# Kernel tuning notes

Measured on AMD Instinct MI355X. Metric: run time of the kernel, lower is better.

The kernel has to match this reference:

```python
import jax, jax.numpy as jnp
import numpy as np
import math

ATTN_SCALE = 1.0 / math.sqrt(128.0)
NEG_INF = float(np.finfo(np.float32).min)


def get_slopes(n_heads: int) -> np.ndarray:
    # ALiBi head-specific slopes, geometric series; handles non-power-of-2 heads.
    n = 2 ** math.floor(math.log2(n_heads))
    m_0 = 2.0 ** (-8.0 / n)
    m = m_0 ** np.arange(1, 1 + n, dtype=np.float64)
    if n < n_heads:
        m_hat_0 = 2.0 ** (-4.0 / n)
        m_hat = m_hat_0 ** np.arange(1, 1 + 2 * (n_heads - n), 2, dtype=np.float64)
        m = np.concatenate([m, m_hat])
    return m.astype(np.float32).reshape(1, -1, 1, 1)  # [1, h, 1, 1]


def setup_inputs() -> dict:
    key = jax.random.key(0)
    kq, kk, kv = jax.random.split(key, 3)
    b, h, s, d = 4, 16, 2048, 128
    q = jax.random.normal(kq, (b, h, s, d), dtype=jnp.float32)
    k = jax.random.normal(kk, (b, h, s, d), dtype=jnp.float32)
    v = jax.random.normal(kv, (b, h, s, d), dtype=jnp.float32)
    return {"q": q, "k": k, "v": v}


def reference(q, k, v):
    b, h, s_q, d = q.shape
    s_kv = k.shape[2]
    # scores: [b, h, s_q, s_kv]
    s = jnp.einsum('bhqd,bhkd->bhqk', q, k) * ATTN_SCALE
    # ALiBi: (j - i) * slope_h, added after scaling
    rel = (jnp.arange(s_kv, dtype=q.dtype)[None, :]
           - jnp.arange(s_q, dtype=q.dtype)[:, None])  # [s_q, s_kv]
    slopes = jnp.asarray(get_slopes(h), dtype=q.dtype)  # [1, h, 1, 1]
    s = s + rel[None, None, :, :] * slopes
    # causal mask: positions j > i get -inf
    causal = jnp.arange(s_kv)[None, :] > jnp.arange(s_q)[:, None]  # [s_q, s_kv]
    s = jnp.where(causal[None, None, :, :], jnp.array(-jnp.inf, dtype=s.dtype), s)
    p = jax.nn.softmax(s, axis=-1)
    o = jnp.einsum('bhqk,bhkd->bhqd', p, v)
    return o
```

## Files before the change

kernel.cpp:

```cpp
#include <hip/hip_runtime.h>
#include <math.h>

#define S_LEN 2048
#define DHEAD 128
#define NHEAD 16
#define QBLK  256
#define KVBLK 64
#define ATT_SCALE 0.08838834764831845f
#define LOG2E 1.4426950408889634f
#define SHIFT2 11.5f

#define KP 136
#define VP 72

typedef __attribute__((ext_vector_type(4))) float f32x4;
typedef __attribute__((ext_vector_type(8))) short s16x8;
typedef __attribute__((ext_vector_type(2))) int   i32x2;

__device__ __forceinline__ int pk2(float lo, float hi) {
  int d;
  asm("v_cvt_pk_bf16_f32 %0, %1, %2" : "=v"(d) : "v"(lo), "v"(hi));
  return d;
}

#define BARRIER() do {                                   \
    asm volatile("s_waitcnt lgkmcnt(0)" ::: "memory");   \
    __builtin_amdgcn_s_barrier();                        \
  } while (0)


__global__ __launch_bounds__(512, 2)
void alibi_attn_fwd(const float* __restrict__ Qg, const float* __restrict__ Kg,
                    const float* __restrict__ Vg, float* __restrict__ Og)
{
  __shared__ __align__(16) short kt[2][KVBLK * KP];
  __shared__ __align__(16) short vt[2][DHEAD * VP];

  const int tid  = threadIdx.x;
  const int lane = tid & 63;
  const int w    = tid >> 6;
  const int l16  = lane & 15;
  const int lg   = lane >> 4;

  const int n    = blockIdx.x;
  const int bh   = n & 63;
  const int p    = n >> 6;
  const int head = bh & (NHEAD - 1);

  const size_t base = (size_t)bh * S_LEN * DHEAD;
  const float* Q = Qg + base;
  const float* K = Kg + base;
  const float* V = Vg + base;
  float*       O = Og + base;

  const float slope2 = exp2f(-0.5f * (float)(head + 1)) * LOG2E;
  float cn16[4], rsv[4];
  #pragma unroll
  for (int x = 0; x < 4; ++x) { cn16[x] = (float)(16 * x) * slope2; rsv[x] = (float)x * slope2; }

  s16x8 ones;
  #pragma unroll
  for (int jj = 0; jj < 8; ++jj) ones[jj] = (short)0x3f80;

  const f32x4 zero4 = {0.f, 0.f, 0.f, 0.f};

  const int qt0 = 7 - p, qt1 = p;
  const int qb0 = qt0 * QBLK, qb1 = qt1 * QBLK;
  const int n0  = 4 * (qt0 + 1);
  const int NT  = n0 + 4 * (qt1 + 1);

  const int kr  = tid >> 3;
  const int d0k = 16 * (tid & 7);
  const int grp = tid & 15, vnt = grp >> 2, vg = grp & 3;
  const int Rv  = 16 * vnt + 4 * vg;
  const int dv  = 4 * (tid >> 4);
  const int vslotb = 32 * (vnt >> 1) + 8 * vg + 4 * (vnt & 1);

  f32x4 ka[4], va[4];

#define LOAD_TILE(KV0) do {                                            \
    const float* kp_ = K + (size_t)((KV0) + kr) * DHEAD + d0k;         \
    ka[0] = *(const f32x4*)(kp_);      ka[1] = *(const f32x4*)(kp_ + 4);  \
    ka[2] = *(const f32x4*)(kp_ + 8);  ka[3] = *(const f32x4*)(kp_ + 12); \
    const float* vp_ = V + (size_t)((KV0) + Rv) * DHEAD + dv;          \
    va[0] = *(const f32x4*)(vp_);                                      \
    va[1] = *(const f32x4*)(vp_ + DHEAD);                              \
    va[2] = *(const f32x4*)(vp_ + 2*DHEAD);                            \
    va[3] = *(const f32x4*)(vp_ + 3*DHEAD);                            \
  } while (0)

#define STORE_TILE(B) do {                                             \
    short* ktp = &kt[B][kr * KP + d0k];                                \
    union { int d[4]; s16x8 v; } u0, u1;                               \
    u0.d[0] = pk2(ka[0][0], ka[0][1]); u0.d[1] = pk2(ka[0][2], ka[0][3]); \
    u0.d[2] = pk2(ka[1][0], ka[1][1]); u0.d[3] = pk2(ka[1][2], ka[1][3]); \
    u1.d[0] = pk2(ka[2][0], ka[2][1]); u1.d[1] = pk2(ka[2][2], ka[2][3]); \
    u1.d[2] = pk2(ka[3][0], ka[3][1]); u1.d[3] = pk2(ka[3][2], ka[3][3]); \
    *(s16x8*)(ktp)     = u0.v;                                         \
    *(s16x8*)(ktp + 8) = u1.v;                                         \
    _Pragma("unroll")                                                  \
    for (int e = 0; e < 4; ++e) {                                      \
      i32x2 dvv;                                                       \
      dvv[0] = pk2(va[0][e], va[1][e]);                                \
      dvv[1] = pk2(va[2][e], va[3][e]);                                \
      *(i32x2*)&vt[B][(dv + e) * VP + vslotb] = dvv;                   \
    }                                                                  \
  } while (0)

  s16x8 qf[2][4];
  f32x4 oacc[2][8], lacc[2];
  int   iq0 = 0;
  int   qb  = qb0;

  auto init_phase = [&](int qbn) {
    qb  = qbn;
    iq0 = qbn + 32 * w + l16;
    #pragma unroll
    for (int m = 0; m < 2; ++m) {
      const float* qp = Q + (size_t)(qbn + 32*w + 16*m + l16) * DHEAD + 8*lg;
      #pragma unroll
      for (int c = 0; c < 4; ++c) {
        f32x4 a = *(const f32x4*)(qp + 32*c);
        f32x4 b = *(const f32x4*)(qp + 32*c + 4);
        const float sc = ATT_SCALE * LOG2E;
        union { int d[4]; s16x8 v; } uu;
        uu.d[0] = pk2(a[0]*sc, a[1]*sc); uu.d[1] = pk2(a[2]*sc, a[3]*sc);
        uu.d[2] = pk2(b[0]*sc, b[1]*sc); uu.d[3] = pk2(b[2]*sc, b[3]*sc);
        qf[m][c] = uu.v;
      }
      #pragma unroll
      for (int dt = 0; dt < 8; ++dt) oacc[m][dt] = zero4;
      lacc[m] = zero4;
    }
  };

  auto epilogue = [&](int qbn) {
    #pragma unroll
    for (int m = 0; m < 2; ++m) {
      #pragma unroll
      for (int r = 0; r < 4; ++r) {
        const float inv = 1.0f / lacc[m][r];
        float* op = O + (size_t)(qbn + 32*w + 16*m + 4*lg + r) * DHEAD + l16;
        #pragma unroll
        for (int dt = 0; dt < 8; ++dt) op[dt * 16] = oacc[m][dt][r] * inv;
      }
    }
  };

  init_phase(qb0);
  LOAD_TILE(0);
  STORE_TILE(0);
  LOAD_TILE(KVBLK);
  __syncthreads();

  for (int s = 0; s < NT; ++s) {
    if (s == n0) { epilogue(qb0); init_phase(qb1); }
    const int cur = s & 1;
    const int kv0 = ((s < n0) ? s : s - n0) * KVBLK;
    const bool active = (kv0 <= qb + 32 * w + 31);
    const short* ktc = kt[cur];
    const short* vtc = vt[cur];

    f32x4 sacc[2][4];
    if (active) {
      #pragma unroll
      for (int nt = 0; nt < 4; ++nt) { sacc[0][nt] = zero4; sacc[1][nt] = zero4; }
      __builtin_amdgcn_s_setprio(1);
      #pragma unroll
      for (int c = 0; c < 4; ++c) {
        #pragma unroll
        for (int nt = 0; nt < 4; ++nt) {
          s16x8 kf = *(const s16x8*)&ktc[(nt*16 + l16) * KP + 32*c + 8*lg];
          sacc[0][nt] = __builtin_amdgcn_mfma_f32_16x16x32_bf16(kf, qf[0][c], sacc[0][nt], 0, 0, 0);
          sacc[1][nt] = __builtin_amdgcn_mfma_f32_16x16x32_bf16(kf, qf[1][c], sacc[1][nt], 0, 0, 0);
        }
      }
      __builtin_amdgcn_s_setprio(0);
    }

    if (s + 1 < NT) STORE_TILE((s + 1) & 1);
    if (s + 2 < NT) {
      const int s2 = s + 2;
      LOAD_TILE(((s2 < n0) ? s2 : s2 - n0) * KVBLK);
    }

    if (active) {
      const bool needMask = (kv0 + KVBLK - 1 > qb + 32 * w);
      s16x8 pa[2][2];
      #pragma unroll
      for (int m = 0; m < 2; ++m) {
        const int dji = kv0 + 4*lg - (iq0 + 16*m);
        const float b0m = (float)dji * slope2 - SHIFT2;
        float pv[4][4];
        #pragma unroll
        for (int nt = 0; nt < 4; ++nt) {
          const float bmn = b0m + cn16[nt];
          #pragma unroll
          for (int r = 0; r < 4; ++r)
            pv[nt][r] = __builtin_amdgcn_exp2f(sacc[m][nt][r] + bmn + rsv[r]);
        }
        if (needMask) {
          #pragma unroll
          for (int nt = 0; nt < 4; ++nt)
            #pragma unroll
            for (int r = 0; r < 4; ++r)
              if (dji + 16*nt + r > 0) pv[nt][r] = 0.f;
        }
        #pragma unroll
        for (int c2 = 0; c2 < 2; ++c2) {
          union { int d[4]; s16x8 v; } uu;
          uu.d[0] = pk2(pv[2*c2][0],   pv[2*c2][1]);
          uu.d[1] = pk2(pv[2*c2][2],   pv[2*c2][3]);
          uu.d[2] = pk2(pv[2*c2+1][0], pv[2*c2+1][1]);
          uu.d[3] = pk2(pv[2*c2+1][2], pv[2*c2+1][3]);
          pa[m][c2] = uu.v;
        }
      }

      __builtin_amdgcn_s_setprio(1);
      #pragma unroll
      for (int c2 = 0; c2 < 2; ++c2) {
        lacc[0] = __builtin_amdgcn_mfma_f32_16x16x32_bf16(pa[0][c2], ones, lacc[0], 0, 0, 0);
        lacc[1] = __builtin_amdgcn_mfma_f32_16x16x32_bf16(pa[1][c2], ones, lacc[1], 0, 0, 0);
        #pragma unroll
        for (int dt = 0; dt < 8; ++dt) {
          s16x8 bv = *(const s16x8*)&vtc[(dt*16 + l16) * VP + c2*32 + 8*lg];
          oacc[0][dt] = __builtin_amdgcn_mfma_f32_16x16x32_bf16(pa[0][c2], bv, oacc[0][dt], 0, 0, 0);
          oacc[1][dt] = __builtin_amdgcn_mfma_f32_16x16x32_bf16(pa[1][c2], bv, oacc[1][dt], 0, 0, 0);
        }
      }
      __builtin_amdgcn_s_setprio(0);
    }

    BARRIER();
  }
  epilogue(qb1);
}

extern "C" void kernel_launch(void* const* d_in, const int* in_sizes, int n_in,
                              void* d_out, int out_size, void* d_ws, size_t ws_size,
                              hipStream_t stream) {
  (void)in_sizes; (void)n_in; (void)out_size; (void)d_ws; (void)ws_size;
  const float* q = (const float*)d_in[0];
  const float* k = (const float*)d_in[1];
  const float* v = (const float*)d_in[2];
  float* o = (float*)d_out;
  dim3 grid(256);
  dim3 block(512);
  alibi_attn_fwd<<<grid, block, 0, stream>>>(q, k, v, o);
}
```

Baseline: 110.1 us.

## Software-pipeline PV matmul one tile behind QK with triple-buffered V

Defers the P·V MFMA block for tile s-1 until after the QK and exp computation for tile s, so the MFMA work of one stage can overlap the exp/convert VALU work of the next. V shared memory moves from double to triple buffering to keep the previous tile's V alive, and the shared-memory store of the next tile now happens at the start of each iteration. The extra V buffer raises LDS use and carried P fragments raise register pressure, which may affect the two-blocks-per-CU occupancy target.

```diff
diff --git a/kernel.cpp b/kernel.cpp
--- a/kernel.cpp
+++ b/kernel.cpp
@@ -34,7 +34,7 @@
                     const float* __restrict__ Vg, float* __restrict__ Og)
 {
   __shared__ __align__(16) short kt[2][KVBLK * KP];
-  __shared__ __align__(16) short vt[2][DHEAD * VP];
+  __shared__ __align__(16) short vt[3][DHEAD * VP];
 
   const int tid  = threadIdx.x;
   const int lane = tid & 63;
@@ -89,8 +89,8 @@
     va[3] = *(const f32x4*)(vp_ + 3*DHEAD);                            \
   } while (0)
 
-#define STORE_TILE(B) do {                                             \
-    short* ktp = &kt[B][kr * KP + d0k];                                \
+#define STORE_TILE(BK, BV) do {                                        \
+    short* ktp = &kt[BK][kr * KP + d0k];                               \
     union { int d[4]; s16x8 v; } u0, u1;                               \
     u0.d[0] = pk2(ka[0][0], ka[0][1]); u0.d[1] = pk2(ka[0][2], ka[0][3]); \
     u0.d[2] = pk2(ka[1][0], ka[1][1]); u0.d[3] = pk2(ka[1][2], ka[1][3]); \
@@ -103,7 +103,7 @@
       i32x2 dvv;                                                       \
       dvv[0] = pk2(va[0][e], va[1][e]);                                \
       dvv[1] = pk2(va[2][e], va[3][e]);                                \
-      *(i32x2*)&vt[B][(dv + e) * VP + vslotb] = dvv;                   \
+      *(i32x2*)&vt[BV][(dv + e) * VP + vslotb] = dvv;                  \
     }                                                                  \
   } while (0)
 
@@ -147,22 +147,48 @@
     }
   };
 
+  s16x8 pa[2][2];
+  bool  pactive = false;
+
+  auto pv_block = [&](const short* vtc) {
+    __builtin_amdgcn_s_setprio(1);
+    #pragma unroll
+    for (int c2 = 0; c2 < 2; ++c2) {
+      lacc[0] = __builtin_amdgcn_mfma_f32_16x16x32_bf16(pa[0][c2], ones, lacc[0], 0, 0, 0);
+      lacc[1] = __builtin_amdgcn_mfma_f32_16x16x32_bf16(pa[1][c2], ones, lacc[1], 0, 0, 0);
+      #pragma unroll
+      for (int dt = 0; dt < 8; ++dt) {
+        s16x8 bv = *(const s16x8*)&vtc[(dt*16 + l16) * VP + c2*32 + 8*lg];
+        oacc[0][dt] = __builtin_amdgcn_mfma_f32_16x16x32_bf16(pa[0][c2], bv, oacc[0][dt], 0, 0, 0);
+        oacc[1][dt] = __builtin_amdgcn_mfma_f32_16x16x32_bf16(pa[1][c2], bv, oacc[1][dt], 0, 0, 0);
+      }
+    }
+    __builtin_amdgcn_s_setprio(0);
+  };
+
   init_phase(qb0);
   LOAD_TILE(0);
-  STORE_TILE(0);
+  STORE_TILE(0, 0);
   LOAD_TILE(KVBLK);
   __syncthreads();
 
   for (int s = 0; s < NT; ++s) {
-    if (s == n0) { epilogue(qb0); init_phase(qb1); }
-    const int cur = s & 1;
+    if (s == n0) {
+      if (pactive) pv_block(vt[(n0 - 1) % 3]);
+      epilogue(qb0);
+      init_phase(qb1);
+      pactive = false;
+    }
     const int kv0 = ((s < n0) ? s : s - n0) * KVBLK;
+
+    if (s + 1 < NT) STORE_TILE((s + 1) & 1, (s + 1) % 3);
+
     const bool active = (kv0 <= qb + 32 * w + 31);
-    const short* ktc = kt[cur];
-    const short* vtc = vt[cur];
 
     f32x4 sacc[2][4];
+    s16x8 pnew[2][2];
     if (active) {
+      const short* ktc = kt[s & 1];
       #pragma unroll
       for (int nt = 0; nt < 4; ++nt) { sacc[0][nt] = zero4; sacc[1][nt] = zero4; }
       __builtin_amdgcn_s_setprio(1);
@@ -176,17 +202,8 @@
         }
       }
       __builtin_amdgcn_s_setprio(0);
-    }
-
-    if (s + 1 < NT) STORE_TILE((s + 1) & 1);
-    if (s + 2 < NT) {
-      const int s2 = s + 2;
-      LOAD_TILE(((s2 < n0) ? s2 : s2 - n0) * KVBLK);
-    }
-
-    if (active) {
+
       const bool needMask = (kv0 + KVBLK - 1 > qb + 32 * w);
-      s16x8 pa[2][2];
       #pragma unroll
       for (int m = 0; m < 2; ++m) {
         const int dji = kv0 + 4*lg - (iq0 + 16*m);
@@ -213,27 +230,30 @@
           uu.d[1] = pk2(pv[2*c2][2],   pv[2*c2][3]);
           uu.d[2] = pk2(pv[2*c2+1][0], pv[2*c2+1][1]);
           uu.d[3] = pk2(pv[2*c2+1][2], pv[2*c2+1][3]);
-          pa[m][c2] = uu.v;
-        }
-      }
-
-      __builtin_amdgcn_s_setprio(1);
-      #pragma unroll
-      for (int c2 = 0; c2 < 2; ++c2) {
-        lacc[0] = __builtin_amdgcn_mfma_f32_16x16x32_bf16(pa[0][c2], ones, lacc[0], 0, 0, 0);
-        lacc[1] = __builtin_amdgcn_mfma_f32_16x16x32_bf16(pa[1][c2], ones, lacc[1], 0, 0, 0);
-        #pragma unroll
-        for (int dt = 0; dt < 8; ++dt) {
-          s16x8 bv = *(const s16x8*)&vtc[(dt*16 + l16) * VP + c2*32 + 8*lg];
-          oacc[0][dt] = __builtin_amdgcn_mfma_f32_16x16x32_bf16(pa[0][c2], bv, oacc[0][dt], 0, 0, 0);
-          oacc[1][dt] = __builtin_amdgcn_mfma_f32_16x16x32_bf16(pa[1][c2], bv, oacc[1][dt], 0, 0, 0);
-        }
-      }
-      __builtin_amdgcn_s_setprio(0);
+          pnew[m][c2] = uu.v;
+        }
+      }
+    }
+
+    if (pactive) pv_block(vt[(s - 1) % 3]);
+
+    if (active) {
+      #pragma unroll
+      for (int m = 0; m < 2; ++m)
+        #pragma unroll
+        for (int c2 = 0; c2 < 2; ++c2) pa[m][c2] = pnew[m][c2];
+    }
+    pactive = active;
+
+    if (s + 2 < NT) {
+      const int s2 = s + 2;
+      LOAD_TILE(((s2 < n0) ? s2 : s2 - n0) * KVBLK);
     }
 
     BARRIER();
   }
+
+  if (pactive) pv_block(vt[(NT - 1) % 3]);
   epilogue(qb1);
 }
 
```

Result: no change. 109.0 us (-1.0%).

## Quad-buffer KV tiles, two tiles per barrier, interleave warp query rows

Applied to the files above, without the earlier changes.

Grows the K/V shared-memory ring from two to four buffers and processes two KV tiles per barrier, which halves the number of block-wide synchronisations. Each global prefetch is issued ahead of the compute for the tile before it. Each warp's two 16-row query slices are now spread 128 rows apart instead of adjacent, and each slice is skipped separately when it lies fully above the causal diagonal. The aim is to balance causal work across warps and cut barrier stalls. The cost is roughly double the LDS footprint per block, which may limit occupancy to one block per CU.

```diff
diff --git a/kernel.cpp b/kernel.cpp
--- a/kernel.cpp
+++ b/kernel.cpp
@@ -33,8 +33,8 @@
 void alibi_attn_fwd(const float* __restrict__ Qg, const float* __restrict__ Kg,
                     const float* __restrict__ Vg, float* __restrict__ Og)
 {
-  __shared__ __align__(16) short kt[2][KVBLK * KP];
-  __shared__ __align__(16) short vt[2][DHEAD * VP];
+  __shared__ __align__(16) short kt[4][KVBLK * KP];
+  __shared__ __align__(16) short vt[4][DHEAD * VP];
 
   const int tid  = threadIdx.x;
   const int lane = tid & 63;
@@ -68,6 +68,7 @@
   const int qb0 = qt0 * QBLK, qb1 = qt1 * QBLK;
   const int n0  = 4 * (qt0 + 1);
   const int NT  = n0 + 4 * (qt1 + 1);
+  const int NP  = NT >> 1;
 
   const int kr  = tid >> 3;
   const int d0k = 16 * (tid & 7);
@@ -77,6 +78,8 @@
   const int vslotb = 32 * (vnt >> 1) + 8 * vg + 4 * (vnt & 1);
 
   f32x4 ka[4], va[4];
+
+#define TKV(T) ((((T) < n0) ? (T) : (T) - n0) * KVBLK)
 
 #define LOAD_TILE(KV0) do {                                            \
     const float* kp_ = K + (size_t)((KV0) + kr) * DHEAD + d0k;         \
@@ -109,15 +112,13 @@
 
   s16x8 qf[2][4];
   f32x4 oacc[2][8], lacc[2];
-  int   iq0 = 0;
-  int   qb  = qb0;
+  int   rowb[2];
 
   auto init_phase = [&](int qbn) {
-    qb  = qbn;
-    iq0 = qbn + 32 * w + l16;
     #pragma unroll
     for (int m = 0; m < 2; ++m) {
-      const float* qp = Q + (size_t)(qbn + 32*w + 16*m + l16) * DHEAD + 8*lg;
+      rowb[m] = qbn + 16 * (w + 8 * m);
+      const float* qp = Q + (size_t)(rowb[m] + l16) * DHEAD + 8*lg;
       #pragma unroll
       for (int c = 0; c < 4; ++c) {
         f32x4 a = *(const f32x4*)(qp + 32*c);
@@ -134,107 +135,111 @@
     }
   };
 
-  auto epilogue = [&](int qbn) {
+  auto epilogue = [&]() {
     #pragma unroll
     for (int m = 0; m < 2; ++m) {
       #pragma unroll
       for (int r = 0; r < 4; ++r) {
         const float inv = 1.0f / lacc[m][r];
-        float* op = O + (size_t)(qbn + 32*w + 16*m + 4*lg + r) * DHEAD + l16;
+        float* op = O + (size_t)(rowb[m] + 4*lg + r) * DHEAD + l16;
         #pragma unroll
         for (int dt = 0; dt < 8; ++dt) op[dt * 16] = oacc[m][dt][r] * inv;
       }
     }
   };
 
-  init_phase(qb0);
-  LOAD_TILE(0);
-  STORE_TILE(0);
-  LOAD_TILE(KVBLK);
-  __syncthreads();
-
-  for (int s = 0; s < NT; ++s) {
-    if (s == n0) { epilogue(qb0); init_phase(qb1); }
-    const int cur = s & 1;
-    const int kv0 = ((s < n0) ? s : s - n0) * KVBLK;
-    const bool active = (kv0 <= qb + 32 * w + 31);
-    const short* ktc = kt[cur];
-    const short* vtc = vt[cur];
+  auto compute = [&](int t) {
+    const int kv0 = TKV(t);
+    const bool act0 = (kv0 <= rowb[0] + 15);
+    const bool act1 = (kv0 <= rowb[1] + 15);
+    if (!(act0 || act1)) return;
+    const short* ktc = kt[t & 3];
+    const short* vtc = vt[t & 3];
 
     f32x4 sacc[2][4];
-    if (active) {
-      #pragma unroll
-      for (int nt = 0; nt < 4; ++nt) { sacc[0][nt] = zero4; sacc[1][nt] = zero4; }
-      __builtin_amdgcn_s_setprio(1);
-      #pragma unroll
-      for (int c = 0; c < 4; ++c) {
+    #pragma unroll
+    for (int nt = 0; nt < 4; ++nt) { sacc[0][nt] = zero4; sacc[1][nt] = zero4; }
+    __builtin_amdgcn_s_setprio(1);
+    #pragma unroll
+    for (int c = 0; c < 4; ++c) {
+      #pragma unroll
+      for (int nt = 0; nt < 4; ++nt) {
+        s16x8 kf = *(const s16x8*)&ktc[(nt*16 + l16) * KP + 32*c + 8*lg];
+        if (act0) sacc[0][nt] = __builtin_amdgcn_mfma_f32_16x16x32_bf16(kf, qf[0][c], sacc[0][nt], 0, 0, 0);
+        if (act1) sacc[1][nt] = __builtin_amdgcn_mfma_f32_16x16x32_bf16(kf, qf[1][c], sacc[1][nt], 0, 0, 0);
+      }
+    }
+    __builtin_amdgcn_s_setprio(0);
+
+    s16x8 pa[2][2];
+    #pragma unroll
+    for (int m = 0; m < 2; ++m) {
+      const bool actm = m ? act1 : act0;
+      if (!actm) continue;
+      const int dji = kv0 + 4*lg - (rowb[m] + l16);
+      const bool needMask = (kv0 + KVBLK - 1 > rowb[m]);
+      const float b0m = (float)dji * slope2 - SHIFT2;
+      float pv[4][4];
+      #pragma unroll
+      for (int nt = 0; nt < 4; ++nt) {
+        const float bmn = b0m + cn16[nt];
         #pragma unroll
-        for (int nt = 0; nt < 4; ++nt) {
-          s16x8 kf = *(const s16x8*)&ktc[(nt*16 + l16) * KP + 32*c + 8*lg];
-          sacc[0][nt] = __builtin_amdgcn_mfma_f32_16x16x32_bf16(kf, qf[0][c], sacc[0][nt], 0, 0, 0);
-          sacc[1][nt] = __builtin_amdgcn_mfma_f32_16x16x32_bf16(kf, qf[1][c], sacc[1][nt], 0, 0, 0);
-        }
-      }
-      __builtin_amdgcn_s_setprio(0);
-    }
-
-    if (s + 1 < NT) STORE_TILE((s + 1) & 1);
-    if (s + 2 < NT) {
-      const int s2 = s + 2;
-      LOAD_TILE(((s2 < n0) ? s2 : s2 - n0) * KVBLK);
-    }
-
-    if (active) {
-      const bool needMask = (kv0 + KVBLK - 1 > qb + 32 * w);
-      s16x8 pa[2][2];
-      #pragma unroll
-      for (int m = 0; m < 2; ++m) {
-        const int dji = kv0 + 4*lg - (iq0 + 16*m);
-        const float b0m = (float)dji * slope2 - SHIFT2;
-        float pv[4][4];
+        for (int r = 0; r < 4; ++r)
+          pv[nt][r] = __builtin_amdgcn_exp2f(sacc[m][nt][r] + bmn + rsv[r]);
+      }
+      if (needMask) {
         #pragma unroll
-        for (int nt = 0; nt < 4; ++nt) {
-          const float bmn = b0m + cn16[nt];
+        for (int nt = 0; nt < 4; ++nt)
           #pragma unroll
           for (int r = 0; r < 4; ++r)
-            pv[nt][r] = __builtin_amdgcn_exp2f(sacc[m][nt][r] + bmn + rsv[r]);
-        }
-        if (needMask) {
-          #pragma unroll
-          for (int nt = 0; nt < 4; ++nt)
-            #pragma unroll
-            for (int r = 0; r < 4; ++r)
-              if (dji + 16*nt + r > 0) pv[nt][r] = 0.f;
-        }
-        #pragma unroll
-        for (int c2 = 0; c2 < 2; ++c2) {
-          union { int d[4]; s16x8 v; } uu;
-          uu.d[0] = pk2(pv[2*c2][0],   pv[2*c2][1]);
-          uu.d[1] = pk2(pv[2*c2][2],   pv[2*c2][3]);
-          uu.d[2] = pk2(pv[2*c2+1][0], pv[2*c2+1][1]);
-          uu.d[3] = pk2(pv[2*c2+1][2], pv[2*c2+1][3]);
-          pa[m][c2] = uu.v;
-        }
-      }
-
-      __builtin_amdgcn_s_setprio(1);
+            if (dji + 16*nt + r > 0) pv[nt][r] = 0.f;
+      }
       #pragma unroll
       for (int c2 = 0; c2 < 2; ++c2) {
-        lacc[0] = __builtin_amdgcn_mfma_f32_16x16x32_bf16(pa[0][c2], ones, lacc[0], 0, 0, 0);
-        lacc[1] = __builtin_amdgcn_mfma_f32_16x16x32_bf16(pa[1][c2], ones, lacc[1], 0, 0, 0);
-        #pragma unroll
-        for (int dt = 0; dt < 8; ++dt) {
-          s16x8 bv = *(const s16x8*)&vtc[(dt*16 + l16) * VP + c2*32 + 8*lg];
-          oacc[0][dt] = __builtin_amdgcn_mfma_f32_16x16x32_bf16(pa[0][c2], bv, oacc[0][dt], 0, 0, 0);
-          oacc[1][dt] = __builtin_amdgcn_mfma_f32_16x16x32_bf16(pa[1][c2], bv, oacc[1][dt], 0, 0, 0);
-        }
-      }
-      __builtin_amdgcn_s_setprio(0);
-    }
+        union { int d[4]; s16x8 v; } uu;
+        uu.d[0] = pk2(pv[2*c2][0],   pv[2*c2][1]);
+        uu.d[1] = pk2(pv[2*c2][2],   pv[2*c2][3]);
+        uu.d[2] = pk2(pv[2*c2+1][0], pv[2*c2+1][1]);
+        uu.d[3] = pk2(pv[2*c2+1][2], pv[2*c2+1][3]);
+        pa[m][c2] = uu.v;
+      }
+    }
+
+    __builtin_amdgcn_s_setprio(1);
+    #pragma unroll
+    for (int c2 = 0; c2 < 2; ++c2) {
+      if (act0) lacc[0] = __builtin_amdgcn_mfma_f32_16x16x32_bf16(pa[0][c2], ones, lacc[0], 0, 0, 0);
+      if (act1) lacc[1] = __builtin_amdgcn_mfma_f32_16x16x32_bf16(pa[1][c2], ones, lacc[1], 0, 0, 0);
+      #pragma unroll
+      for (int dt = 0; dt < 8; ++dt) {
+        s16x8 bv = *(const s16x8*)&vtc[(dt*16 + l16) * VP + c2*32 + 8*lg];
+        if (act0) oacc[0][dt] = __builtin_amdgcn_mfma_f32_16x16x32_bf16(pa[0][c2], bv, oacc[0][dt], 0, 0, 0);
+        if (act1) oacc[1][dt] = __builtin_amdgcn_mfma_f32_16x16x32_bf16(pa[1][c2], bv, oacc[1][dt], 0, 0, 0);
+      }
+    }
+    __builtin_amdgcn_s_setprio(0);
+  };
+
+  init_phase(qb0);
+  LOAD_TILE(TKV(0));  STORE_TILE(0);
+  LOAD_TILE(TKV(1));  STORE_TILE(1);
+  LOAD_TILE(TKV(2));
+  __syncthreads();
+
+  for (int per = 0; per < NP; ++per) {
+    const int t0 = 2 * per, t1 = t0 + 1;
+    if (t0 == n0) { epilogue(); init_phase(qb1); }
+
+    if (t0 + 2 < NT) STORE_TILE((t0 + 2) & 3);
+    if (t0 + 3 < NT) LOAD_TILE(TKV(t0 + 3));
+    compute(t0);
+    if (t0 + 3 < NT) STORE_TILE((t0 + 3) & 3);
+    if (t0 + 4 < NT) LOAD_TILE(TKV(t0 + 4));
+    compute(t1);
 
     BARRIER();
   }
-  epilogue(qb1);
+  epilogue();
 }
 
 extern "C" void kernel_launch(void* const* d_in, const int* in_sizes, int n_in,
```

After: 122.2 us. 11.0% more time.
